# Kernel tuning notes

Hardware: AMD Instinct MI355X
Metric: run time of the kernel (lower is better)

## Reference

```python
import jax, jax.numpy as jnp
import numpy as np

DIM = 1024
NUM_HEADS = 16


def setup_inputs() -> dict:
    key = jax.random.key(0)
    ks = jax.random.split(key, 6)
    B, N, C = 2, 2048, DIM
    input_qv = jax.random.normal(ks[0], (B, N, C), dtype=jnp.float32)
    input_k = jax.random.normal(ks[1], (B, N, C), dtype=jnp.float32)
    # Linear weights stored [in, out]; qkv_bias=False so qv/k have no bias.
    s = 1.0 / np.sqrt(C)
    W_qv = jax.random.uniform(ks[2], (C, 2 * C), dtype=jnp.float32, minval=-s, maxval=s)
    W_k = jax.random.uniform(ks[3], (C, C), dtype=jnp.float32, minval=-s, maxval=s)
    W_proj = jax.random.uniform(ks[4], (C, C), dtype=jnp.float32, minval=-s, maxval=s)
    b_proj = jax.random.uniform(ks[5], (C,), dtype=jnp.float32, minval=-s, maxval=s)
    return {"input_qv": input_qv, "input_k": input_k, "W_qv": W_qv,
            "W_k": W_k, "W_proj": W_proj, "b_proj": b_proj}


def reference(input_qv, input_k, W_qv, W_k, W_proj, b_proj):
    B, N, C = input_qv.shape
    H = NUM_HEADS
    Dh = C // H
    scale = Dh ** -0.5
    # qv projection -> [B, N, 2, H, Dh] -> q, v each [B, H, N, Dh]
    qv = (input_qv @ W_qv).reshape(B, N, 2, H, Dh)
    q = jnp.transpose(qv[:, :, 0], (0, 2, 1, 3))  # [B, H, N, Dh]
    v = jnp.transpose(qv[:, :, 1], (0, 2, 1, 3))  # [B, H, N, Dh]
    k = jnp.transpose((input_k @ W_k).reshape(B, N, H, Dh), (0, 2, 1, 3))  # [B, H, N, Dh]
    # explicit QK^T softmax V (dropout ratio 0 -> identity)
    atten = jnp.einsum('bhnd,bhmd->bhnm', q, k) * scale  # [B, H, N, N]
    atten = jax.nn.softmax(atten, axis=-1)
    x = jnp.einsum('bhnm,bhmd->bhnd', atten, v)  # [B, H, N, Dh]
    x = jnp.transpose(x, (0, 2, 1, 3)).reshape(B, N, C)
    return x @ W_proj + b_proj
```

## Files before the change

kernel.cpp:

```cpp
#include <hip/hip_runtime.h>
#include <stdint.h>

#define BATCH 2
#define SEQ   2048
#define DIM   1024
#define NH    16
#define DH    64

typedef short bf16x8 __attribute__((ext_vector_type(8)));
typedef float floatx4 __attribute__((ext_vector_type(4)));

__device__ __forceinline__ int swz(int r) { return (r ^ (r >> 2)) & 3; }

#if __has_builtin(__builtin_amdgcn_exp2f)
#define EXP2(x) __builtin_amdgcn_exp2f(x)
#else
#define EXP2(x) __expf((x) * 0.6931471805599453f)
#endif

__device__ __forceinline__ uint32_t pack_bf16_rne(float x0, float x1) {
    uint32_t u0 = __float_as_uint(x0), u1 = __float_as_uint(x1);
    u0 += 0x7FFFu + ((u0 >> 16) & 1);
    u1 += 0x7FFFu + ((u1 >> 16) & 1);
    return (u0 >> 16) | (u1 & 0xFFFF0000u);
}

__device__ __forceinline__ ushort bf16_rne1(float x) {
    uint32_t u = __float_as_uint(x);
    u += 0x7FFFu + ((u >> 16) & 1);
    return (ushort)(u >> 16);
}

#define KSCALE 0.18033688011112042f

__global__ __launch_bounds__(256, 3)
void gemm_qvk(const float* __restrict__ Aqv, const float* __restrict__ Akp,
              const float* __restrict__ Wqv, const float* __restrict__ Wkp,
              uint32_t* __restrict__ qh, ushort* __restrict__ vt,
              uint32_t* __restrict__ kh)
{
    __shared__ uint32_t Ah[2][128 * 16], Bh[2][128 * 16];

    const int t    = threadIdx.x;
    const int lane = t & 63;
    const int w    = t >> 6;
    const int wm   = w & 1, wn = w >> 1;
    const int quad = lane >> 4, l15 = lane & 15;
    const int bx   = blockIdx.x;
    const bool is_qv = (bx < 16);
    const float* Af = is_qv ? Aqv : Akp;
    const float* Bf = is_qv ? Wqv : Wkp;
    const int N    = is_qv ? 2048 : 1024;
    const int n0   = (is_qv ? bx : bx - 16) * 128;
    const int m0   = blockIdx.y * 128;

    const int ar  = t >> 1;
    const int ab0 = (t & 1) * 2;
    const int as  = swz(ar);
    const int bc  = (t & 31) * 4;
    const int bk  = (t >> 5) * 4;
    const int bb  = bk >> 3;
    const int bp  = (bk & 7) >> 1;
    const bool nsel = ((bc >> 4) & 1) != 0;

    floatx4 acc[4][4];
    #pragma unroll
    for (int i = 0; i < 4; i++)
        #pragma unroll
        for (int j = 0; j < 4; j++)
            #pragma unroll
            for (int e = 0; e < 4; e++) acc[i][j][e] = 0.0f;

    float f0[16], f1[16];
    float4 g40[4], g41[4];
    {
        #pragma unroll
        for (int i = 0; i < 4; i++) {
            *(float4*)&f0[i * 4] =
                *(const float4*)&Af[(size_t)(m0 + ar) * 1024 + ab0 * 8 + i * 4];
            *(float4*)&f1[i * 4] =
                *(const float4*)&Af[(size_t)(m0 + ar) * 1024 + 32 + ab0 * 8 + i * 4];
        }
        #pragma unroll
        for (int j = 0; j < 4; j++) {
            g40[j] = *(const float4*)&Bf[(size_t)(bk + j) * N + n0 + bc];
            g41[j] = *(const float4*)&Bf[(size_t)(32 + bk + j) * N + n0 + bc];
        }
    }

    for (int k0 = 0; k0 < 1024; k0 += 64) {
        if (k0) __syncthreads();
        {
            uint32_t hi[8];
            #pragma unroll
            for (int j = 0; j < 8; j++) hi[j] = pack_bf16_rne(f0[2 * j], f0[2 * j + 1]);
            int i0 = ar * 16 + ((ab0 ^ as) * 4);
            int i1 = ar * 16 + (((ab0 + 1) ^ as) * 4);
            *(uint4*)&Ah[0][i0] = make_uint4(hi[0], hi[1], hi[2], hi[3]);
            *(uint4*)&Ah[0][i1] = make_uint4(hi[4], hi[5], hi[6], hi[7]);
            #pragma unroll
            for (int j = 0; j < 8; j++) hi[j] = pack_bf16_rne(f1[2 * j], f1[2 * j + 1]);
            *(uint4*)&Ah[1][i0] = make_uint4(hi[0], hi[1], hi[2], hi[3]);
            *(uint4*)&Ah[1][i1] = make_uint4(hi[4], hi[5], hi[6], hi[7]);
        }
        {
            #pragma unroll
            for (int i = 0; i < 4; i++) {
                int n = bc + (i ^ (nsel ? 1 : 0));
                int bi = n * 16 + ((bb ^ swz(n)) * 4) + bp;
                float e0 = nsel ? ((const float*)&g40[0])[i ^ 1] : ((const float*)&g40[0])[i];
                float e1 = nsel ? ((const float*)&g40[1])[i ^ 1] : ((const float*)&g40[1])[i];
                float e2 = nsel ? ((const float*)&g40[2])[i ^ 1] : ((const float*)&g40[2])[i];
                float e3 = nsel ? ((const float*)&g40[3])[i ^ 1] : ((const float*)&g40[3])[i];
                *(uint2*)&Bh[0][bi] = make_uint2(pack_bf16_rne(e0, e1), pack_bf16_rne(e2, e3));
                e0 = nsel ? ((const float*)&g41[0])[i ^ 1] : ((const float*)&g41[0])[i];
                e1 = nsel ? ((const float*)&g41[1])[i ^ 1] : ((const float*)&g41[1])[i];
                e2 = nsel ? ((const float*)&g41[2])[i ^ 1] : ((const float*)&g41[2])[i];
                e3 = nsel ? ((const float*)&g41[3])[i ^ 1] : ((const float*)&g41[3])[i];
                *(uint2*)&Bh[1][bi] = make_uint2(pack_bf16_rne(e0, e1), pack_bf16_rne(e2, e3));
            }
        }
        __syncthreads();

        if (k0 + 64 < 1024) {
            #pragma unroll
            for (int i = 0; i < 4; i++) {
                *(float4*)&f0[i * 4] =
                    *(const float4*)&Af[(size_t)(m0 + ar) * 1024 + (k0 + 64) + ab0 * 8 + i * 4];
                *(float4*)&f1[i * 4] =
                    *(const float4*)&Af[(size_t)(m0 + ar) * 1024 + (k0 + 96) + ab0 * 8 + i * 4];
            }
            #pragma unroll
            for (int j = 0; j < 4; j++) {
                g40[j] = *(const float4*)&Bf[(size_t)(k0 + 64 + bk + j) * N + n0 + bc];
                g41[j] = *(const float4*)&Bf[(size_t)(k0 + 96 + bk + j) * N + n0 + bc];
            }
        }

        #pragma unroll
        for (int half = 0; half < 2; half++) {
            bf16x8 vb[4];
            #pragma unroll
            for (int fn = 0; fn < 4; fn++) {
                int br = wn * 64 + fn * 16 + l15;
                int bi = br * 16 + ((quad ^ swz(br)) * 4);
                vb[fn] = *(const bf16x8*)&Bh[half][bi];
            }
            #pragma unroll
            for (int fm = 0; fm < 4; fm++) {
                int arow = wm * 64 + fm * 16 + l15;
                int ai = arow * 16 + ((quad ^ swz(arow)) * 4);
                bf16x8 va = *(const bf16x8*)&Ah[half][ai];
                #pragma unroll
                for (int fn = 0; fn < 4; fn++)
                    acc[fm][fn] = __builtin_amdgcn_mfma_f32_16x16x32_bf16(vb[fn], va, acc[fm][fn], 0, 0, 0);
            }
        }
    }

    #pragma unroll
    for (int fm = 0; fm < 4; fm++) {
        int row = m0 + wm * 64 + fm * 16 + l15;
        #pragma unroll
        for (int fn = 0; fn < 4; fn++) {
            int colb = n0 + wn * 64 + fn * 16 + quad * 4;
            floatx4 a = acc[fm][fn];
            if (is_qv) {
                if (colb < 1024) {
                    uint32_t u0 = pack_bf16_rne(a[0], a[1]);
                    uint32_t u1 = pack_bf16_rne(a[2], a[3]);
                    size_t wi = (size_t)row * 512 + (colb >> 1);
                    *(uint2*)&qh[wi] = make_uint2(u0, u1);
                } else {
                    int hh = (colb - 1024) >> 6;
                    int d0 = (colb - 1024) & 63;
                    #pragma unroll
                    for (int j = 0; j < 4; j++)
                        vt[(size_t)(hh * 64 + d0 + j) * 4096 + row] = bf16_rne1(a[j]);
                }
            } else {
                uint32_t u0 = pack_bf16_rne(a[0] * KSCALE, a[1] * KSCALE);
                uint32_t u1 = pack_bf16_rne(a[2] * KSCALE, a[3] * KSCALE);
                size_t wi = (size_t)row * 512 + (colb >> 1);
                *(uint2*)&kh[wi] = make_uint2(u0, u1);
            }
        }
    }
}

__global__ __launch_bounds__(256, 3)
void gemm_projB(const uint32_t* __restrict__ Ag,
                const float* __restrict__ Bf, const float* __restrict__ bias,
                float* __restrict__ Cf, float* __restrict__ P1)
{
    __shared__ uint32_t Ah[2][128 * 16], Bh[2][128 * 16];

    const int t    = threadIdx.x;
    const int lane = t & 63;
    const int w    = t >> 6;
    const int wm   = w & 1, wn = w >> 1;
    const int quad = lane >> 4, l15 = lane & 15;
    const int m0 = blockIdx.y * 128, n0 = blockIdx.x * 128;
    const int kz = blockIdx.z;
    const int k0 = kz * 512;
    const int N  = 1024;

    const int bc  = (t & 31) * 4;
    const int bk  = (t >> 5) * 4;
    const int bb  = bk >> 3;
    const int bp  = (bk & 7) >> 1;
    const bool nsel = ((bc >> 4) & 1) != 0;

    const int arow0 = t >> 2, akbl = t & 3;
    const int arow1 = (t + 256) >> 2;
    const int dst0 = arow0 * 16 + ((akbl ^ swz(arow0)) * 4);
    const int dst1 = arow1 * 16 + ((akbl ^ swz(arow1)) * 4);

    floatx4 acc[4][4];
    #pragma unroll
    for (int i = 0; i < 4; i++)
        #pragma unroll
        for (int j = 0; j < 4; j++)
            #pragma unroll
            for (int e = 0; e < 4; e++) acc[i][j][e] = 0.0f;

    uint4 gA00, gA01, gA10, gA11;
    float4 g40[4], g41[4];
    {
        size_t s0 = (size_t)(m0 + arow0) * 512 + (k0 >> 1) + akbl * 4;
        size_t s1 = (size_t)(m0 + arow1) * 512 + (k0 >> 1) + akbl * 4;
        gA00 = *(const uint4*)&Ag[s0];
        gA01 = *(const uint4*)&Ag[s1];
        gA10 = *(const uint4*)&Ag[s0 + 16];
        gA11 = *(const uint4*)&Ag[s1 + 16];
        #pragma unroll
        for (int j = 0; j < 4; j++) {
            g40[j] = *(const float4*)&Bf[(size_t)(k0 + bk + j) * N + n0 + bc];
            g41[j] = *(const float4*)&Bf[(size_t)(k0 + 32 + bk + j) * N + n0 + bc];
        }
    }

    for (int kk = 0; kk < 512; kk += 64) {
        if (kk) __syncthreads();
        {
            *(uint4*)&Ah[0][dst0] = gA00;
            *(uint4*)&Ah[0][dst1] = gA01;
            *(uint4*)&Ah[1][dst0] = gA10;
            *(uint4*)&Ah[1][dst1] = gA11;
        }
        {
            #pragma unroll
            for (int i = 0; i < 4; i++) {
                int n = bc + (i ^ (nsel ? 1 : 0));
                int bi = n * 16 + ((bb ^ swz(n)) * 4) + bp;
                float e0 = nsel ? ((const float*)&g40[0])[i ^ 1] : ((const float*)&g40[0])[i];
                float e1 = nsel ? ((const float*)&g40[1])[i ^ 1] : ((const float*)&g40[1])[i];
                float e2 = nsel ? ((const float*)&g40[2])[i ^ 1] : ((const float*)&g40[2])[i];
                float e3 = nsel ? ((const float*)&g40[3])[i ^ 1] : ((const float*)&g40[3])[i];
                *(uint2*)&Bh[0][bi] = make_uint2(pack_bf16_rne(e0, e1), pack_bf16_rne(e2, e3));
                e0 = nsel ? ((const float*)&g41[0])[i ^ 1] : ((const float*)&g41[0])[i];
                e1 = nsel ? ((const float*)&g41[1])[i ^ 1] : ((const float*)&g41[1])[i];
                e2 = nsel ? ((const float*)&g41[2])[i ^ 1] : ((const float*)&g41[2])[i];
                e3 = nsel ? ((const float*)&g41[3])[i ^ 1] : ((const float*)&g41[3])[i];
                *(uint2*)&Bh[1][bi] = make_uint2(pack_bf16_rne(e0, e1), pack_bf16_rne(e2, e3));
            }
        }
        __syncthreads();

        if (kk + 64 < 512) {
            const int kg = k0 + kk + 64;
            size_t s0 = (size_t)(m0 + arow0) * 512 + (kg >> 1) + akbl * 4;
            size_t s1 = (size_t)(m0 + arow1) * 512 + (kg >> 1) + akbl * 4;
            gA00 = *(const uint4*)&Ag[s0];
            gA01 = *(const uint4*)&Ag[s1];
            gA10 = *(const uint4*)&Ag[s0 + 16];
            gA11 = *(const uint4*)&Ag[s1 + 16];
            #pragma unroll
            for (int j = 0; j < 4; j++) {
                g40[j] = *(const float4*)&Bf[(size_t)(kg + bk + j) * N + n0 + bc];
                g41[j] = *(const float4*)&Bf[(size_t)(kg + 32 + bk + j) * N + n0 + bc];
            }
        }

        #pragma unroll
        for (int half = 0; half < 2; half++) {
            bf16x8 vb[4];
            #pragma unroll
            for (int fn = 0; fn < 4; fn++) {
                int br = wn * 64 + fn * 16 + l15;
                int bi = br * 16 + ((quad ^ swz(br)) * 4);
                vb[fn] = *(const bf16x8*)&Bh[half][bi];
            }
            #pragma unroll
            for (int fm = 0; fm < 4; fm++) {
                int arow = wm * 64 + fm * 16 + l15;
                int ai = arow * 16 + ((quad ^ swz(arow)) * 4);
                bf16x8 va = *(const bf16x8*)&Ah[half][ai];
                #pragma unroll
                for (int fn = 0; fn < 4; fn++)
                    acc[fm][fn] = __builtin_amdgcn_mfma_f32_16x16x32_bf16(vb[fn], va, acc[fm][fn], 0, 0, 0);
            }
        }
    }

    #pragma unroll
    for (int fm = 0; fm < 4; fm++) {
        int row = m0 + wm * 64 + fm * 16 + l15;
        #pragma unroll
        for (int fn = 0; fn < 4; fn++) {
            int colb = n0 + wn * 64 + fn * 16 + quad * 4;
            floatx4 a = acc[fm][fn];
            float4 v;
            if (kz == 0) {
                float4 bb4 = *(const float4*)&bias[colb];
                v.x = a[0] + bb4.x; v.y = a[1] + bb4.y;
                v.z = a[2] + bb4.z; v.w = a[3] + bb4.w;
                *(float4*)&Cf[(size_t)row * N + colb] = v;
            } else {
                v.x = a[0]; v.y = a[1]; v.z = a[2]; v.w = a[3];
                *(float4*)&P1[(size_t)row * N + colb] = v;
            }
        }
    }
}

__global__ __launch_bounds__(256)
void add_partial(const float4* __restrict__ p1, float4* __restrict__ out, int n4)
{
    int i = blockIdx.x * 256 + threadIdx.x;
    int stride = gridDim.x * 256;
    for (; i < n4; i += stride) {
        float4 a = out[i];
        float4 b = p1[i];
        a.x += b.x; a.y += b.y; a.z += b.z; a.w += b.w;
        out[i] = a;
    }
}

#define FST 34
#define FSV 66
#define FSP 66
#define NT  (SEQ / 128)
__global__ __launch_bounds__(256, 2)
void flash_attn(const uint32_t* __restrict__ qhg,
                const uint32_t* __restrict__ khg,
                const uint32_t* __restrict__ vtg,
                uint32_t* __restrict__ xhg)
{
    __shared__ uint32_t Kh[128 * FST];
    __shared__ uint32_t Vt[64 * FSV];
    __shared__ uint32_t Pt[128 * FSP];

    const int t    = threadIdx.x;
    const int lane = t & 63;
    const int w    = t >> 6;
    const int quad = lane >> 4, l15 = lane & 15;
    const int qb = blockIdx.x;
    const int h  = blockIdx.y;
    const int b  = blockIdx.z;

    const size_t rowbase = (size_t)b * SEQ;

    bf16x8 vq[2][2];
    {
        #pragma unroll
        for (int nf = 0; nf < 2; nf++) {
            size_t row = rowbase + qb * 128 + w * 32 + nf * 16 + l15;
            size_t gw = row * 512 + h * 32 + quad * 4;
            #pragma unroll
            for (int s = 0; s < 2; s++)
                vq[s][nf] = *(const bf16x8*)&qhg[gw + s * 16];
        }
    }

    const int kr  = t >> 1, kc0 = (t & 1) * 16;
    const int vd = t >> 2, vc = t & 3;
    const size_t vrow = (size_t)(h * 64 + vd) * 2048 + (rowbase >> 1);
    uint4 pk0, pk1, pk2, pk3, pv0, pv1, pv2, pv3;
    {
        size_t gw = (rowbase + kr) * 512 + h * 32 + kc0;
        pk0 = *(const uint4*)&khg[gw];
        pk1 = *(const uint4*)&khg[gw + 4];
        pk2 = *(const uint4*)&khg[gw + 8];
        pk3 = *(const uint4*)&khg[gw + 12];
        size_t vw = vrow + vc * 16;
        pv0 = *(const uint4*)&vtg[vw];
        pv1 = *(const uint4*)&vtg[vw + 4];
        pv2 = *(const uint4*)&vtg[vw + 8];
        pv3 = *(const uint4*)&vtg[vw + 12];
    }

    float m_i[2] = {-INFINITY, -INFINITY};
    float l_i[2] = {0.0f, 0.0f};
    floatx4 acc_o[2][4];
    #pragma unroll
    for (int nf = 0; nf < 2; nf++)
        #pragma unroll
        for (int fm = 0; fm < 4; fm++)
            #pragma unroll
            for (int e = 0; e < 4; e++) acc_o[nf][fm][e] = 0.0f;

    for (int kt = 0; kt < NT; kt++) {
        __syncthreads();
        {
            int kb0 = kr * FST + kc0;
            *(uint4*)&Kh[kb0]      = pk0;
            *(uint4*)&Kh[kb0 + 4]  = pk1;
            *(uint4*)&Kh[kb0 + 8]  = pk2;
            *(uint4*)&Kh[kb0 + 12] = pk3;
        }
        {
            int vb0 = vd * FSV + vc * 16;
            *(uint2*)&Vt[vb0]      = make_uint2(pv0.x, pv0.y);
            *(uint2*)&Vt[vb0 + 2]  = make_uint2(pv0.z, pv0.w);
            *(uint2*)&Vt[vb0 + 4]  = make_uint2(pv1.x, pv1.y);
            *(uint2*)&Vt[vb0 + 6]  = make_uint2(pv1.z, pv1.w);
            *(uint2*)&Vt[vb0 + 8]  = make_uint2(pv2.x, pv2.y);
            *(uint2*)&Vt[vb0 + 10] = make_uint2(pv2.z, pv2.w);
            *(uint2*)&Vt[vb0 + 12] = make_uint2(pv3.x, pv3.y);
            *(uint2*)&Vt[vb0 + 14] = make_uint2(pv3.z, pv3.w);
        }
        __syncthreads();

        if (kt + 1 < NT) {
            size_t gw = (rowbase + (kt + 1) * 128 + kr) * 512 + h * 32 + kc0;
            pk0 = *(const uint4*)&khg[gw];
            pk1 = *(const uint4*)&khg[gw + 4];
            pk2 = *(const uint4*)&khg[gw + 8];
            pk3 = *(const uint4*)&khg[gw + 12];
            size_t vw = vrow + (kt + 1) * 64 + vc * 16;
            pv0 = *(const uint4*)&vtg[vw];
            pv1 = *(const uint4*)&vtg[vw + 4];
            pv2 = *(const uint4*)&vtg[vw + 8];
            pv3 = *(const uint4*)&vtg[vw + 12];
        }

        floatx4 sacc[2][8];
        #pragma unroll
        for (int nf = 0; nf < 2; nf++)
            #pragma unroll
            for (int fm = 0; fm < 8; fm++)
                #pragma unroll
                for (int e = 0; e < 4; e++) sacc[nf][fm][e] = 0.0f;

        __builtin_amdgcn_s_setprio(1);
        #pragma unroll
        for (int s = 0; s < 2; s++) {
            #pragma unroll
            for (int fm = 0; fm < 8; fm++) {
                int ki = (fm * 16 + l15) * FST + s * 16 + quad * 4;
                bf16x8 vk = *(const bf16x8*)&Kh[ki];
                #pragma unroll
                for (int nf = 0; nf < 2; nf++)
                    sacc[nf][fm] = __builtin_amdgcn_mfma_f32_16x16x32_bf16(vk, vq[s][nf], sacc[nf][fm], 0, 0, 0);
            }
        }
        __builtin_amdgcn_s_setprio(0);

        #pragma unroll
        for (int nf = 0; nf < 2; nf++) {
            float mt = -INFINITY;
            #pragma unroll
            for (int fm = 0; fm < 8; fm++)
                #pragma unroll
                for (int r = 0; r < 4; r++) mt = fmaxf(mt, sacc[nf][fm][r]);
            mt = fmaxf(mt, __shfl_xor(mt, 16));
            mt = fmaxf(mt, __shfl_xor(mt, 32));

            if (__all(mt - m_i[nf] <= 8.0f)) {
                float rs = 0.0f;
                #pragma unroll
                for (int fm = 0; fm < 8; fm++)
                    #pragma unroll
                    for (int r = 0; r < 4; r++) {
                        sacc[nf][fm][r] = EXP2(sacc[nf][fm][r] - m_i[nf]);
                        rs += sacc[nf][fm][r];
                    }
                rs += __shfl_xor(rs, 16);
                rs += __shfl_xor(rs, 32);
                l_i[nf] += rs;
            } else {
                float m_new = fmaxf(m_i[nf], mt);
                float alpha = EXP2(m_i[nf] - m_new);
                float rs = 0.0f;
                #pragma unroll
                for (int fm = 0; fm < 8; fm++)
                    #pragma unroll
                    for (int r = 0; r < 4; r++) {
                        sacc[nf][fm][r] = EXP2(sacc[nf][fm][r] - m_new);
                        rs += sacc[nf][fm][r];
                    }
                rs += __shfl_xor(rs, 16);
                rs += __shfl_xor(rs, 32);
                l_i[nf] = l_i[nf] * alpha + rs;
                m_i[nf] = m_new;
                #pragma unroll
                for (int fm = 0; fm < 4; fm++)
                    #pragma unroll
                    for (int e = 0; e < 4; e++) acc_o[nf][fm][e] *= alpha;
            }

            int qrow = w * 32 + nf * 16 + l15;
            #pragma unroll
            for (int fm = 0; fm < 8; fm++) {
                uint32_t u0 = pack_bf16_rne(sacc[nf][fm][0], sacc[nf][fm][1]);
                uint32_t u1 = pack_bf16_rne(sacc[nf][fm][2], sacc[nf][fm][3]);
                *(uint2*)&Pt[qrow * FSP + fm * 8 + quad * 2] = make_uint2(u0, u1);
            }
        }

        __builtin_amdgcn_s_setprio(1);
        #pragma unroll
        for (int s = 0; s < 4; s++) {
            bf16x8 pb[2];
            #pragma unroll
            for (int nf = 0; nf < 2; nf++)
                pb[nf] = *(const bf16x8*)&Pt[(w * 32 + nf * 16 + l15) * FSP + s * 16 + quad * 4];
            #pragma unroll
            for (int fm = 0; fm < 4; fm++) {
                bf16x8 va = *(const bf16x8*)&Vt[(fm * 16 + l15) * FSV + s * 16 + quad * 4];
                #pragma unroll
                for (int nf = 0; nf < 2; nf++)
                    acc_o[nf][fm] = __builtin_amdgcn_mfma_f32_16x16x32_bf16(va, pb[nf], acc_o[nf][fm], 0, 0, 0);
            }
        }
        __builtin_amdgcn_s_setprio(0);
    }

    #pragma unroll
    for (int nf = 0; nf < 2; nf++) {
        float rl = 1.0f / l_i[nf];
        size_t row = rowbase + qb * 128 + w * 32 + nf * 16 + l15;
        #pragma unroll
        for (int fm = 0; fm < 4; fm++) {
            int d0 = fm * 16 + quad * 4;
            uint32_t u0 = pack_bf16_rne(acc_o[nf][fm][0] * rl, acc_o[nf][fm][1] * rl);
            uint32_t u1 = pack_bf16_rne(acc_o[nf][fm][2] * rl, acc_o[nf][fm][3] * rl);
            size_t wi = row * 512 + ((h * 64 + d0) >> 1);
            *(uint2*)&xhg[wi] = make_uint2(u0, u1);
        }
    }
}

extern "C" void kernel_launch(void* const* d_in, const int* in_sizes, int n_in,
                              void* d_out, int out_size, void* d_ws, size_t ws_size,
                              hipStream_t stream)
{
    const float* input_qv = (const float*)d_in[0];
    const float* input_k  = (const float*)d_in[1];
    const float* W_qv     = (const float*)d_in[2];
    const float* W_k      = (const float*)d_in[3];
    const float* W_proj   = (const float*)d_in[4];
    const float* b_proj   = (const float*)d_in[5];
    float* out = (float*)d_out;

    const size_t RW = 4096 * 512;
    uint32_t* qh = (uint32_t*)d_ws;
    uint32_t* vt = qh + RW;
    uint32_t* xh = vt + RW;
    uint32_t* kh = (uint32_t*)d_out;
    float* p1 = (float*)d_ws;

    dim3 blk(256);
    gemm_qvk<<<dim3(24, 32), blk, 0, stream>>>(
        input_qv, input_k, W_qv, W_k, qh, (ushort*)vt, kh);
    flash_attn<<<dim3(SEQ / 128, NH, BATCH), blk, 0, stream>>>(
        qh, kh, vt, xh);
    gemm_projB<<<dim3(8, 32, 2), blk, 0, stream>>>(
        xh, W_proj, b_proj, out, p1);
    add_partial<<<dim3(2048), blk, 0, stream>>>(
        (const float4*)p1, (float4*)out, 4096 * 1024 / 4);
}
```

Measured before the change: 244.8 us.

## Read V fragments directly from global memory and swizzle GEMM block order

```diff
diff --git a/kernel.cpp b/kernel.cpp
--- a/kernel.cpp
+++ b/kernel.cpp
@@ -46,13 +46,18 @@
     const int w    = t >> 6;
     const int wm   = w & 1, wn = w >> 1;
     const int quad = lane >> 4, l15 = lane & 15;
-    const int bx   = blockIdx.x;
-    const bool is_qv = (bx < 16);
+
+    const int lin = blockIdx.y * 24 + blockIdx.x;
+    const int sl  = (lin & 7) * 96 + (lin >> 3);
+    const int bxs = sl % 24;
+    const int bys = sl / 24;
+
+    const bool is_qv = (bxs < 16);
     const float* Af = is_qv ? Aqv : Akp;
     const float* Bf = is_qv ? Wqv : Wkp;
     const int N    = is_qv ? 2048 : 1024;
-    const int n0   = (is_qv ? bx : bx - 16) * 128;
-    const int m0   = blockIdx.y * 128;
+    const int n0   = (is_qv ? bxs : bxs - 16) * 128;
+    const int m0   = bys * 128;
 
     const int ar  = t >> 1;
     const int ab0 = (t & 1) * 2;
@@ -200,8 +205,14 @@
     const int w    = t >> 6;
     const int wm   = w & 1, wn = w >> 1;
     const int quad = lane >> 4, l15 = lane & 15;
-    const int m0 = blockIdx.y * 128, n0 = blockIdx.x * 128;
-    const int kz = blockIdx.z;
+
+    const int lin = blockIdx.z * 256 + blockIdx.y * 8 + blockIdx.x;
+    const int sl  = (lin & 7) * 64 + (lin >> 3);
+    const int bxs = sl & 7;
+    const int bys = (sl >> 3) & 31;
+    const int kz  = sl >> 8;
+
+    const int m0 = bys * 128, n0 = bxs * 128;
     const int k0 = kz * 512;
     const int N  = 1024;
 
@@ -338,17 +349,15 @@
 }
 
 #define FST 34
-#define FSV 66
 #define FSP 66
 #define NT  (SEQ / 128)
-__global__ __launch_bounds__(256, 2)
+__global__ __launch_bounds__(256, 3)
 void flash_attn(const uint32_t* __restrict__ qhg,
                 const uint32_t* __restrict__ khg,
                 const uint32_t* __restrict__ vtg,
                 uint32_t* __restrict__ xhg)
 {
     __shared__ uint32_t Kh[128 * FST];
-    __shared__ uint32_t Vt[64 * FSV];
     __shared__ uint32_t Pt[128 * FSP];
 
     const int t    = threadIdx.x;
@@ -374,21 +383,16 @@
     }
 
     const int kr  = t >> 1, kc0 = (t & 1) * 16;
-    const int vd = t >> 2, vc = t & 3;
-    const size_t vrow = (size_t)(h * 64 + vd) * 2048 + (rowbase >> 1);
-    uint4 pk0, pk1, pk2, pk3, pv0, pv1, pv2, pv3;
+    uint4 pk0, pk1, pk2, pk3;
     {
         size_t gw = (rowbase + kr) * 512 + h * 32 + kc0;
         pk0 = *(const uint4*)&khg[gw];
         pk1 = *(const uint4*)&khg[gw + 4];
         pk2 = *(const uint4*)&khg[gw + 8];
         pk3 = *(const uint4*)&khg[gw + 12];
-        size_t vw = vrow + vc * 16;
-        pv0 = *(const uint4*)&vtg[vw];
-        pv1 = *(const uint4*)&vtg[vw + 4];
-        pv2 = *(const uint4*)&vtg[vw + 8];
-        pv3 = *(const uint4*)&vtg[vw + 12];
-    }
+    }
+
+    const size_t vbl = (size_t)(h * 64 + l15) * 2048 + (rowbase >> 1) + quad * 4;
 
     float m_i[2] = {-INFINITY, -INFINITY};
     float l_i[2] = {0.0f, 0.0f};
@@ -409,17 +413,6 @@
             *(uint4*)&Kh[kb0 + 8]  = pk2;
             *(uint4*)&Kh[kb0 + 12] = pk3;
         }
-        {
-            int vb0 = vd * FSV + vc * 16;
-            *(uint2*)&Vt[vb0]      = make_uint2(pv0.x, pv0.y);
-            *(uint2*)&Vt[vb0 + 2]  = make_uint2(pv0.z, pv0.w);
-            *(uint2*)&Vt[vb0 + 4]  = make_uint2(pv1.x, pv1.y);
-            *(uint2*)&Vt[vb0 + 6]  = make_uint2(pv1.z, pv1.w);
-            *(uint2*)&Vt[vb0 + 8]  = make_uint2(pv2.x, pv2.y);
-            *(uint2*)&Vt[vb0 + 10] = make_uint2(pv2.z, pv2.w);
-            *(uint2*)&Vt[vb0 + 12] = make_uint2(pv3.x, pv3.y);
-            *(uint2*)&Vt[vb0 + 14] = make_uint2(pv3.z, pv3.w);
-        }
         __syncthreads();
 
         if (kt + 1 < NT) {
@@ -428,11 +421,6 @@
             pk1 = *(const uint4*)&khg[gw + 4];
             pk2 = *(const uint4*)&khg[gw + 8];
             pk3 = *(const uint4*)&khg[gw + 12];
-            size_t vw = vrow + (kt + 1) * 64 + vc * 16;
-            pv0 = *(const uint4*)&vtg[vw];
-            pv1 = *(const uint4*)&vtg[vw + 4];
-            pv2 = *(const uint4*)&vtg[vw + 8];
-            pv3 = *(const uint4*)&vtg[vw + 12];
         }
 
         floatx4 sacc[2][8];
@@ -518,7 +506,7 @@
                 pb[nf] = *(const bf16x8*)&Pt[(w * 32 + nf * 16 + l15) * FSP + s * 16 + quad * 4];
             #pragma unroll
             for (int fm = 0; fm < 4; fm++) {
-                bf16x8 va = *(const bf16x8*)&Vt[(fm * 16 + l15) * FSV + s * 16 + quad * 4];
+                bf16x8 va = *(const bf16x8*)&vtg[vbl + (size_t)fm * 32768 + kt * 64 + s * 16];
                 #pragma unroll
                 for (int nf = 0; nf < 2; nf++)
                     acc_o[nf][fm] = __builtin_amdgcn_mfma_f32_16x16x32_bf16(va, pb[nf], acc_o[nf][fm], 0, 0, 0);
```

Measured after the change: 317.4 us. 1.3x slower.
